# Optimization experiments

Hardware: AMD Instinct MI355X
Metric: run time of the kernel (lower is better)

Reference implementation:

```python
import jax, jax.numpy as jnp
import numpy as np

N_NODES = 50000
IN_F, HID_F, OUT_F = 256, 128, 40
N_EDGES = 800000


def _uniform(key, shape, scale):
    return jax.random.uniform(key, shape, dtype=jnp.float32, minval=-scale, maxval=scale)


def setup_inputs() -> dict:
    key = jax.random.key(0)
    ks = jax.random.split(key, 20)
    x = jax.random.normal(ks[0], (N_NODES, IN_F), dtype=jnp.float32)
    edge_index = jax.random.randint(ks[1], (2, N_EDGES), 0, N_NODES, dtype=jnp.int64)
    s0, sa0 = 1.0 / np.sqrt(HID_F), 1.0  # std_att = 1/sqrt(1)
    s1, sa1 = 1.0 / np.sqrt(OUT_F), 1.0
    sv = 1.0 / np.sqrt(3.0)
    return {
        "x": x, "edge_index": edge_index,
        "Wl0": _uniform(ks[2], (IN_F, HID_F), s0),
        "Wh0": _uniform(ks[3], (IN_F, HID_F), s0),
        "Wm0": _uniform(ks[4], (IN_F, HID_F), s0),
        "al0": _uniform(ks[5], (HID_F, 1), sa0),
        "ah0": _uniform(ks[6], (HID_F, 1), sa0),
        "am0": _uniform(ks[7], (HID_F, 1), sa0),
        "att0": _uniform(ks[8], (3, 3), sv),
        "Wl1": _uniform(ks[9], (HID_F, OUT_F), s1),
        "Wh1": _uniform(ks[10], (HID_F, OUT_F), s1),
        "Wm1": _uniform(ks[11], (HID_F, OUT_F), s1),
        "al1": _uniform(ks[12], (OUT_F, 1), sa1),
        "ah1": _uniform(ks[13], (OUT_F, 1), sa1),
        "am1": _uniform(ks[14], (OUT_F, 1), sa1),
        "att1": _uniform(ks[15], (3, 3), sv),
    }


def _acm_layer(x, row, col, d_inv, Wl, Wh, Wm, al, ah, am, att):
    n = x.shape[0]
    hl, hh, hm = x @ Wl, x @ Wh, x @ Wm
    # adj_low @ M  with adj_low = D^{-1}(I + A): gather sources, scatter-add to rows
    def low(M):
        return d_inv[:, None] * (M + jax.ops.segment_sum(M[col], row, num_segments=n))
    out_low = jax.nn.relu(low(hl))
    out_high = jax.nn.relu(hh - low(hh))  # adj_high = I - adj_low
    out_mlp = jax.nn.relu(hm)
    T = 3.0
    sig = jax.nn.sigmoid(jnp.concatenate([out_low @ al, out_high @ ah, out_mlp @ am], axis=1))  # [n,3]
    a = jax.nn.softmax((sig @ att) / T, axis=1)
    return 3.0 * (a[:, 0:1] * out_low + a[:, 1:2] * out_high + a[:, 2:3] * out_mlp)


def reference(x, edge_index, Wl0, Wh0, Wm0, al0, ah0, am0, att0,
              Wl1, Wh1, Wm1, al1, ah1, am1, att1):
    n = x.shape[0]
    row, col = edge_index[0], edge_index[1]
    deg = jax.ops.segment_sum(jnp.ones_like(row, dtype=jnp.float32), row, num_segments=n)
    rowsum = 1.0 + deg  # rowsum of I + A (duplicates counted, as in scipy)
    d_inv = jnp.where(rowsum > 0, 1.0 / rowsum, 0.0)
    h = _acm_layer(x, row, col, d_inv, Wl0, Wh0, Wm0, al0, ah0, am0, att0)
    out = _acm_layer(h, row, col, d_inv, Wl1, Wh1, Wm1, al1, ah1, am1, att1)
    return out
```

## Files before the change

kernel.cpp:

```cpp
#include <hip/hip_runtime.h>
#include <math.h>

#define N_NODES 50000
#define N_EDGES 800000
#define IN_F    256
#define HID_F   128
#define OUT_F   40
#define W0N     (3*HID_F)
#define W1N     (3*OUT_F)
#define NB      ((N_NODES + 255) / 256)

#define SEG     128
#define EPB     (N_EDGES / SEG)
#define NWORD   (N_NODES / 2)
#define WB      ((NWORD + 255) / 256)

#define XB   ((N_NODES * IN_F) / (256 * 16))
#define P0B  ((IN_F * W0N) / 256)
#define P1B  ((HID_F * W1N) / 256)
#define PREPB (XB + P0B + P1B)

typedef __attribute__((ext_vector_type(8))) unsigned short ushort8;
typedef __attribute__((ext_vector_type(4))) unsigned short ushort4v;
typedef __attribute__((ext_vector_type(8))) __bf16 bf16x8;
typedef __attribute__((ext_vector_type(4))) float f32x4;
typedef __attribute__((ext_vector_type(2))) float f32x2;

static __device__ __forceinline__ float sigmoidf_(float x) {
    return 1.0f / (1.0f + expf(-x));
}

static __device__ __forceinline__ unsigned short f2bf(float f) {
    unsigned u = __float_as_uint(f);
    u += 0x7FFFu + ((u >> 16) & 1u);
    return (unsigned short)(u >> 16);
}

static __device__ __forceinline__ float bflo(unsigned u) { return __uint_as_float(u << 16); }
static __device__ __forceinline__ float bfhi(unsigned u) { return __uint_as_float(u & 0xffff0000u); }
static __device__ __forceinline__ int rfl(int v) { return __builtin_amdgcn_readfirstlane(v); }


__global__ __launch_bounds__(256) void k_hist(
        const int* __restrict__ ei, unsigned* __restrict__ segHist,
        unsigned short* __restrict__ rank, unsigned* __restrict__ rc) {
    __shared__ unsigned hist[NWORD];
    int t = threadIdx.x, seg = blockIdx.x;
    for (int i = t; i < NWORD; i += 256) hist[i] = 0;
    __syncthreads();
    int base = seg * EPB;
    for (int k = t; k < EPB; k += 256) {
        int e = base + k;
        int r = ei[e];
        int c = ei[N_EDGES + e];
        unsigned old = atomicAdd(&hist[r >> 1], (r & 1) ? 0x10000u : 1u);
        unsigned lr = (r & 1) ? (old >> 16) : (old & 0xffffu);
        rank[e] = (unsigned short)lr;
        rc[e] = ((unsigned)r << 16) | (unsigned)c;
    }
    __syncthreads();
    unsigned* dst = segHist + (size_t)seg * NWORD;
    for (int i = t; i < NWORD; i += 256) dst[i] = hist[i];
}


__global__ __launch_bounds__(256) void k_scanseg(
        unsigned* __restrict__ segHist, int* __restrict__ rowPtr,
        float* __restrict__ dinv, int* __restrict__ blkTot) {
    __shared__ int s[256];
    int t = threadIdx.x;
    int w = blockIdx.x * 256 + t;
    int cum0 = 0, cum1 = 0;
    if (w < NWORD) {
        for (int sg = 0; sg < SEG; ++sg) {
            size_t idx = (size_t)sg * NWORD + w;
            unsigned h = segHist[idx];
            segHist[idx] = ((unsigned)cum1 << 16) | (unsigned)cum0;
            cum0 += (int)(h & 0xffffu);
            cum1 += (int)(h >> 16);
        }
    }
    int deg0 = cum0, deg1 = cum1;
    int pair = deg0 + deg1;
    s[t] = pair; __syncthreads();
    for (int d = 1; d < 256; d <<= 1) {
        int x = (t >= d) ? s[t - d] : 0;
        __syncthreads();
        s[t] += x;
        __syncthreads();
    }
    int basep = s[t] - pair;
    if (w < NWORD) {
        rowPtr[2 * w]     = basep;
        rowPtr[2 * w + 1] = basep + deg0;
        dinv[2 * w]     = 1.0f / (1.0f + (float)deg0);
        dinv[2 * w + 1] = 1.0f / (1.0f + (float)deg1);
    }
    if (t == 255) blkTot[blockIdx.x] = s[255];
}

__global__ void k_scan2(int* __restrict__ blk) {
    __shared__ int s[256];
    int t = threadIdx.x;
    int v = (t < WB) ? blk[t] : 0;
    s[t] = v; __syncthreads();
    for (int d = 1; d < 256; d <<= 1) {
        int x = (t >= d) ? s[t - d] : 0;
        __syncthreads();
        s[t] += x;
        __syncthreads();
    }
    if (t < WB) blk[t] = s[t] - v;
}

__global__ void k_scan3(const int* __restrict__ blkOff, int* __restrict__ rowPtr) {
    int t = threadIdx.x;
    int gid = blockIdx.x * 256 + t;
    if (gid < N_NODES) rowPtr[gid] += blkOff[gid >> 9];
    if (gid == 0) rowPtr[N_NODES] = N_EDGES;
}


__global__ __launch_bounds__(256) void k_prep(
        const float* __restrict__ x, unsigned short* __restrict__ xb,
        const float* __restrict__ Wl0, const float* __restrict__ Wh0,
        const float* __restrict__ Wm0, unsigned short* __restrict__ W0t,
        const float* __restrict__ Wl1, const float* __restrict__ Wh1,
        const float* __restrict__ Wm1, unsigned short* __restrict__ W1t) {
    int b = blockIdx.x, t = threadIdx.x;
    if (b < XB) {
        size_t idx = (size_t)b * 4096 + t * 16;
        float4 f0 = *(const float4*)(x + idx);
        float4 f1 = *(const float4*)(x + idx + 4);
        float4 f2 = *(const float4*)(x + idx + 8);
        float4 f3 = *(const float4*)(x + idx + 12);
        ushort8 u0, u1;
        u0[0]=f2bf(f0.x); u0[1]=f2bf(f0.y); u0[2]=f2bf(f0.z); u0[3]=f2bf(f0.w);
        u0[4]=f2bf(f1.x); u0[5]=f2bf(f1.y); u0[6]=f2bf(f1.z); u0[7]=f2bf(f1.w);
        u1[0]=f2bf(f2.x); u1[1]=f2bf(f2.y); u1[2]=f2bf(f2.z); u1[3]=f2bf(f2.w);
        u1[4]=f2bf(f3.x); u1[5]=f2bf(f3.y); u1[6]=f2bf(f3.z); u1[7]=f2bf(f3.w);
        *(ushort8*)(xb + idx)     = u0;
        *(ushort8*)(xb + idx + 8) = u1;
    } else if (b < XB + P0B) {
        int i = (b - XB) * 256 + t;
        int n = i / IN_F, k = i % IN_F;
        float v;
        if (n < HID_F)            v = Wl0[k * HID_F + n];
        else if (n < 2 * HID_F)   v = Wh0[k * HID_F + (n - HID_F)];
        else                      v = Wm0[k * HID_F + (n - 2 * HID_F)];
        W0t[i] = f2bf(v);
    } else {
        int i = (b - XB - P0B) * 256 + t;
        int n = i / HID_F, kp = i % HID_F;
        int k = ((kp >> 6) << 6) + ((kp & 3) << 4) + ((kp >> 2) & 15);
        float v;
        if (n < OUT_F)            v = Wl1[k * OUT_F + n];
        else if (n < 2 * OUT_F)   v = Wh1[k * OUT_F + (n - OUT_F)];
        else                      v = Wm1[k * OUT_F + (n - 2 * OUT_F)];
        W1t[i] = f2bf(v);
    }
}


#define BKP 40

template<int EPI>
__global__ __launch_bounds__(256) void k_gemm_fill(
        const unsigned short* __restrict__ A, const unsigned short* __restrict__ Bt,
        unsigned short* __restrict__ C0, int ld0,
        unsigned short* __restrict__ C1, int ld1, int nsplit,
        unsigned char* __restrict__ Cq,
        unsigned short* __restrict__ Hs, unsigned char* __restrict__ Hq,
        unsigned short* __restrict__ HmP,
        int M, int N, int K, int nxt,
        const unsigned* __restrict__ rc, const unsigned short* __restrict__ rank,
        const int* __restrict__ rowPtr, const unsigned short* __restrict__ segOff,
        unsigned short* __restrict__ colIdx) {
    __shared__ unsigned short As[128 * BKP];
    __shared__ unsigned short Bs[128 * BKP];
    int tid  = threadIdx.x;

    if ((int)blockIdx.x >= nxt) {
        int fid = (blockIdx.x - nxt) * gridDim.y + blockIdx.y;
        int e = fid * 256 + tid;
        if (e < N_EDGES) {
            unsigned x = rc[e];
            int r = (int)(x >> 16);
            int seg = e / EPB;
            int pos = rowPtr[r] + (int)segOff[(size_t)seg * N_NODES + r] + (int)rank[e];
            colIdx[pos] = (unsigned short)(x & 0xffffu);
        }
        return;
    }

    int lane = tid & 63, wid = tid >> 6;
    int wr = wid >> 1, wc = wid & 1;
    int bm = blockIdx.y * 128, bn = blockIdx.x * 128;

    int srow = tid >> 1;
    int scol = (tid & 1) * 16;

    int garow = min(bm + srow, M - 1);
    int gbrow = min(bn + srow, N - 1);

    f32x4 acc[4][4];
#pragma unroll
    for (int m = 0; m < 4; ++m)
#pragma unroll
        for (int n = 0; n < 4; ++n)
            acc[m][n] = (f32x4)(0.0f);

    int kg = (lane >> 4) * 8;
    int rA = wr * 64 + (lane & 15);
    int rB = wc * 64 + (lane & 15);

    for (int k0 = 0; k0 < K; k0 += 32) {
        {
            const unsigned short* src = A + (size_t)garow * K + k0 + scol;
            *(ushort8*)&As[srow * BKP + scol]     = *(const ushort8*)(src);
            *(ushort8*)&As[srow * BKP + scol + 8] = *(const ushort8*)(src + 8);
        }
        {
            const unsigned short* src = Bt + (size_t)gbrow * K + k0 + scol;
            *(ushort8*)&Bs[srow * BKP + scol]     = *(const ushort8*)(src);
            *(ushort8*)&Bs[srow * BKP + scol + 8] = *(const ushort8*)(src + 8);
        }
        __syncthreads();

        bf16x8 a[4], b[4];
#pragma unroll
        for (int m = 0; m < 4; ++m)
            a[m] = __builtin_bit_cast(bf16x8, *(const ushort8*)&As[(rA + m * 16) * BKP + kg]);
#pragma unroll
        for (int n = 0; n < 4; ++n)
            b[n] = __builtin_bit_cast(bf16x8, *(const ushort8*)&Bs[(rB + n * 16) * BKP + kg]);
#pragma unroll
        for (int m = 0; m < 4; ++m)
#pragma unroll
            for (int n = 0; n < 4; ++n)
                acc[m][n] = __builtin_amdgcn_mfma_f32_16x16x32_bf16(a[m], b[n], acc[m][n], 0, 0, 0);
        __syncthreads();
    }

    int col  = lane & 15;
    int rsub = (lane >> 4) * 4;

    if (EPI == 0) {
#pragma unroll
        for (int m = 0; m < 4; ++m) {
            int gm0 = bm + wr * 64 + m * 16 + rsub;
#pragma unroll
            for (int n = 0; n < 4; ++n) {
                int gn = bn + wc * 64 + n * 16 + col;
                if (gn >= N) continue;
#pragma unroll
                for (int j = 0; j < 4; ++j) {
                    int gm = gm0 + j;
                    if (gm >= M) continue;
                    float v = acc[m][n][j];
                    unsigned short b = f2bf(v);
                    if (gn < nsplit) {
                        C0[(size_t)gm * ld0 + gn] = b;
                        int pk = __builtin_amdgcn_cvt_pk_fp8_f32(v, v, 0, false);
                        Cq[(size_t)gm * nsplit + gn] = (unsigned char)(pk & 0xff);
                    } else {
                        C1[(size_t)gm * ld1 + (gn - nsplit)] = b;
                    }
                }
            }
        }
    } else {
#pragma unroll
        for (int m = 0; m < 4; ++m) {
            int gm0 = bm + wr * 64 + m * 16 + rsub;
#pragma unroll
            for (int j = 0; j < 4; ++j) {
                int gm = gm0 + j;
                if (gm >= M) continue;
                float v0 = acc[m][0][j], v1 = acc[m][1][j];
                float v2 = acc[m][2][j], v3 = acc[m][3][j];
                ushort4v o;
                o[0] = f2bf(v0); o[1] = f2bf(v1); o[2] = f2bf(v2); o[3] = f2bf(v3);
                if (bn < 256) {
                    int pos = bn + wc * 64 + col * 4;
                    *(ushort4v*)&Hs[(size_t)gm * 256 + pos] = o;
                    int pk = 0;
                    pk = __builtin_amdgcn_cvt_pk_fp8_f32(v0, v1, pk, false);
                    pk = __builtin_amdgcn_cvt_pk_fp8_f32(v2, v3, pk, true);
                    *(unsigned*)&Hq[(size_t)gm * 256 + pos] = (unsigned)pk;
                } else {
                    int pos = wc * 64 + col * 4;
                    *(ushort4v*)&HmP[(size_t)gm * 128 + pos] = o;
                }
            }
        }
    }
}


__global__ __launch_bounds__(256) void k_layer0(
        const unsigned short* __restrict__ Hs, const unsigned char* __restrict__ Hq,
        const unsigned short* __restrict__ HmP,
        const int* __restrict__ rowPtr, const unsigned short* __restrict__ colIdx,
        const float* __restrict__ dinv,
        const float* __restrict__ al, const float* __restrict__ ah,
        const float* __restrict__ am, const float* __restrict__ att,
        unsigned short* __restrict__ hout) {
    int lane = threadIdx.x & 63;
    int i = blockIdx.x * 4 + (threadIdx.x >> 6);

    int p0 = rfl(rowPtr[i]);
    int p1 = rfl(rowPtr[i + 1]);
    float a0 = 0.f, a1 = 0.f, a2 = 0.f, a3 = 0.f;
    int off4 = lane * 4;

    auto acc1 = [&](unsigned j) {
        const unsigned char* row = Hq + ((size_t)(j << 8));
        unsigned w = *(const unsigned*)(row + off4);
        f32x2 d0 = __builtin_amdgcn_cvt_pk_f32_fp8((int)w, false);
        f32x2 d1 = __builtin_amdgcn_cvt_pk_f32_fp8((int)w, true);
        a0 += d0.x; a1 += d0.y; a2 += d1.x; a3 += d1.y;
    };

    int p = p0;
    while ((p & 3) != 0 && p < p1) {
        acc1((unsigned)rfl((int)colIdx[p]));
        ++p;
    }
    for (; p + 7 < p1; p += 8) {
        uint2 ca = *(const uint2*)(colIdx + p);
        uint2 cb = *(const uint2*)(colIdx + p + 4);
        unsigned w0 = (unsigned)rfl((int)ca.x);
        unsigned w1 = (unsigned)rfl((int)ca.y);
        unsigned w2 = (unsigned)rfl((int)cb.x);
        unsigned w3 = (unsigned)rfl((int)cb.y);
        acc1(w0 & 0xffffu); acc1(w0 >> 16);
        acc1(w1 & 0xffffu); acc1(w1 >> 16);
        acc1(w2 & 0xffffu); acc1(w2 >> 16);
        acc1(w3 & 0xffffu); acc1(w3 >> 16);
    }
    for (; p + 3 < p1; p += 4) {
        uint2 ca = *(const uint2*)(colIdx + p);
        unsigned w0 = (unsigned)rfl((int)ca.x);
        unsigned w1 = (unsigned)rfl((int)ca.y);
        acc1(w0 & 0xffffu); acc1(w0 >> 16);
        acc1(w1 & 0xffffu); acc1(w1 >> 16);
    }
    for (; p < p1; ++p) {
        acc1((unsigned)rfl((int)colIdx[p]));
    }

    uint2 sv = *(const uint2*)(Hs + (size_t)i * 256 + off4);
    float s0 = bflo(sv.x), s1 = bfhi(sv.x), s2 = bflo(sv.y), s3 = bfhi(sv.y);
    float di = dinv[i];
    float l0 = di * (s0 + a0), l1 = di * (s1 + a1);
    float l2 = di * (s2 + a2), l3 = di * (s3 + a3);

    float ol0 = fmaxf(l0, 0.f), ol1 = fmaxf(l1, 0.f);
    float ol2 = fmaxf(l2, 0.f), ol3 = fmaxf(l3, 0.f);
    float oh0 = fmaxf(s0 - l0, 0.f), oh1 = fmaxf(s1 - l1, 0.f);
    float oh2 = fmaxf(s2 - l2, 0.f), oh3 = fmaxf(s3 - l3, 0.f);

    int c0 = ((lane >> 4) << 6) + (lane & 15);

    float om0 = 0.f, om1 = 0.f, om2 = 0.f, om3 = 0.f;
    float prA, prM = 0.f;
    if (lane < 32) {
        uint2 hv = *(const uint2*)(HmP + (size_t)i * 128 + off4);
        om0 = fmaxf(bflo(hv.x), 0.f); om1 = fmaxf(bfhi(hv.x), 0.f);
        om2 = fmaxf(bflo(hv.y), 0.f); om3 = fmaxf(bfhi(hv.y), 0.f);
        prA = ol0 * al[c0] + ol1 * al[c0 + 16] + ol2 * al[c0 + 32] + ol3 * al[c0 + 48];
        prM = om0 * am[c0] + om1 * am[c0 + 16] + om2 * am[c0 + 32] + om3 * am[c0 + 48];
    } else {
        int ch = c0 - 128;
        prA = oh0 * ah[ch] + oh1 * ah[ch + 16] + oh2 * ah[ch + 32] + oh3 * ah[ch + 48];
    }

#pragma unroll
    for (int d = 1; d < 32; d <<= 1) prA += __shfl_xor(prA, d);
#pragma unroll
    for (int d = 1; d < 32; d <<= 1) prM += __shfl_xor(prM, d);
    float g0 = __shfl(prA, 0);
    float g1 = __shfl(prA, 32);
    float g2 = __shfl(prM, 0);

    float sg0 = sigmoidf_(g0), sg1 = sigmoidf_(g1), sg2 = sigmoidf_(g2);
    const float inv3 = (1.0f / 3.0f);
    float e0 = (sg0 * att[0] + sg1 * att[3] + sg2 * att[6]) * inv3;
    float e1 = (sg0 * att[1] + sg1 * att[4] + sg2 * att[7]) * inv3;
    float e2 = (sg0 * att[2] + sg1 * att[5] + sg2 * att[8]) * inv3;
    float mx = fmaxf(e0, fmaxf(e1, e2));
    float x0 = expf(e0 - mx), x1 = expf(e1 - mx), x2 = expf(e2 - mx);
    float inv = 1.0f / (x0 + x1 + x2);
    float c0f = 3.0f * inv * x0, c1f = 3.0f * inv * x1, c2f = 3.0f * inv * x2;

    int src = lane | 32;
    float th0 = __shfl(oh0, src), th1 = __shfl(oh1, src);
    float th2 = __shfl(oh2, src), th3 = __shfl(oh3, src);

    if (lane < 32) {
        ushort4v o;
        o[0] = f2bf(c0f * ol0 + c1f * th0 + c2f * om0);
        o[1] = f2bf(c0f * ol1 + c1f * th1 + c2f * om1);
        o[2] = f2bf(c0f * ol2 + c1f * th2 + c2f * om2);
        o[3] = f2bf(c0f * ol3 + c1f * th3 + c2f * om3);
        *(ushort4v*)&hout[(size_t)i * 128 + off4] = o;
    }
}


__global__ __launch_bounds__(256) void k_layer1(
        const unsigned short* __restrict__ H1g, const unsigned char* __restrict__ H1q,
        const unsigned short* __restrict__ H1m,
        const int* __restrict__ rowPtr, const unsigned short* __restrict__ colIdx,
        const float* __restrict__ dinv,
        const float* __restrict__ al, const float* __restrict__ ah,
        const float* __restrict__ am, const float* __restrict__ att,
        float* __restrict__ out) {
    int lane = threadIdx.x & 63;
    int i = blockIdx.x * 4 + (threadIdx.x >> 6);

    int p0 = rfl(rowPtr[i]);
    int p1 = rfl(rowPtr[i + 1]);
    float a0 = 0.f, a1 = 0.f, a2 = 0.f, a3 = 0.f;
    int off4 = lane * 4;
    bool active = lane < 20;

    auto acc1 = [&](unsigned j) {
        const unsigned char* row = H1q + (size_t)(j * 80u);
        unsigned w = *(const unsigned*)(row + off4);
        f32x2 d0 = __builtin_amdgcn_cvt_pk_f32_fp8((int)w, false);
        f32x2 d1 = __builtin_amdgcn_cvt_pk_f32_fp8((int)w, true);
        a0 += d0.x; a1 += d0.y; a2 += d1.x; a3 += d1.y;
    };

    if (active) {
        int p = p0;
        while ((p & 3) != 0 && p < p1) {
            acc1((unsigned)rfl((int)colIdx[p]));
            ++p;
        }
        for (; p + 7 < p1; p += 8) {
            uint2 ca = *(const uint2*)(colIdx + p);
            uint2 cb = *(const uint2*)(colIdx + p + 4);
            unsigned w0 = (unsigned)rfl((int)ca.x);
            unsigned w1 = (unsigned)rfl((int)ca.y);
            unsigned w2 = (unsigned)rfl((int)cb.x);
            unsigned w3 = (unsigned)rfl((int)cb.y);
            acc1(w0 & 0xffffu); acc1(w0 >> 16);
            acc1(w1 & 0xffffu); acc1(w1 >> 16);
            acc1(w2 & 0xffffu); acc1(w2 >> 16);
            acc1(w3 & 0xffffu); acc1(w3 >> 16);
        }
        for (; p + 3 < p1; p += 4) {
            uint2 ca = *(const uint2*)(colIdx + p);
            unsigned w0 = (unsigned)rfl((int)ca.x);
            unsigned w1 = (unsigned)rfl((int)ca.y);
            acc1(w0 & 0xffffu); acc1(w0 >> 16);
            acc1(w1 & 0xffffu); acc1(w1 >> 16);
        }
        for (; p < p1; ++p) {
            acc1((unsigned)rfl((int)colIdx[p]));
        }
    }

    float s0 = 0.f, s1 = 0.f, s2 = 0.f, s3 = 0.f;
    if (active) {
        uint2 sv = *(const uint2*)(H1g + (size_t)i * 80 + off4);
        s0 = bflo(sv.x); s1 = bfhi(sv.x); s2 = bflo(sv.y); s3 = bfhi(sv.y);
    }
    float di = dinv[i];
    float l0 = di * (s0 + a0), l1 = di * (s1 + a1);
    float l2 = di * (s2 + a2), l3 = di * (s3 + a3);

    float ol0 = fmaxf(l0, 0.f), ol1 = fmaxf(l1, 0.f);
    float ol2 = fmaxf(l2, 0.f), ol3 = fmaxf(l3, 0.f);
    float oh0 = fmaxf(s0 - l0, 0.f), oh1 = fmaxf(s1 - l1, 0.f);
    float oh2 = fmaxf(s2 - l2, 0.f), oh3 = fmaxf(s3 - l3, 0.f);

    float om0 = 0.f, om1 = 0.f, om2 = 0.f, om3 = 0.f;
    float r0 = 0.f, r1 = 0.f, r2 = 0.f;
    if (lane < 10) {
        uint2 hv = *(const uint2*)(H1m + (size_t)i * 40 + off4);
        om0 = fmaxf(bflo(hv.x), 0.f); om1 = fmaxf(bfhi(hv.x), 0.f);
        om2 = fmaxf(bflo(hv.y), 0.f); om3 = fmaxf(bfhi(hv.y), 0.f);
        float4 alv = *(const float4*)(al + off4);
        float4 amv = *(const float4*)(am + off4);
        r0 = ol0 * alv.x + ol1 * alv.y + ol2 * alv.z + ol3 * alv.w;
        r2 = om0 * amv.x + om1 * amv.y + om2 * amv.z + om3 * amv.w;
    } else if (lane < 20) {
        float4 ahv = *(const float4*)(ah + (off4 - 40));
        r1 = oh0 * ahv.x + oh1 * ahv.y + oh2 * ahv.z + oh3 * ahv.w;
    }

#pragma unroll
    for (int d = 1; d < 64; d <<= 1) r0 += __shfl_xor(r0, d);
#pragma unroll
    for (int d = 1; d < 64; d <<= 1) r1 += __shfl_xor(r1, d);
#pragma unroll
    for (int d = 1; d < 64; d <<= 1) r2 += __shfl_xor(r2, d);

    float sg0 = sigmoidf_(r0), sg1 = sigmoidf_(r1), sg2 = sigmoidf_(r2);
    const float inv3 = (1.0f / 3.0f);
    float e0 = (sg0 * att[0] + sg1 * att[3] + sg2 * att[6]) * inv3;
    float e1 = (sg0 * att[1] + sg1 * att[4] + sg2 * att[7]) * inv3;
    float e2 = (sg0 * att[2] + sg1 * att[5] + sg2 * att[8]) * inv3;
    float mx = fmaxf(e0, fmaxf(e1, e2));
    float x0 = expf(e0 - mx), x1 = expf(e1 - mx), x2 = expf(e2 - mx);
    float inv = 1.0f / (x0 + x1 + x2);
    float c0 = 3.0f * inv * x0, c1 = 3.0f * inv * x1, c2 = 3.0f * inv * x2;

    int src = (lane + 10) & 63;
    float th0 = __shfl(oh0, src), th1 = __shfl(oh1, src);
    float th2 = __shfl(oh2, src), th3 = __shfl(oh3, src);

    if (lane < 10) {
        float4 o;
        o.x = c0 * ol0 + c1 * th0 + c2 * om0;
        o.y = c0 * ol1 + c1 * th1 + c2 * om1;
        o.z = c0 * ol2 + c1 * th2 + c2 * om2;
        o.w = c0 * ol3 + c1 * th3 + c2 * om3;
        *(float4*)&out[(size_t)i * 40 + off4] = o;
    }
}


extern "C" void kernel_launch(void* const* d_in, const int* in_sizes, int n_in,
                              void* d_out, int out_size, void* d_ws, size_t ws_size,
                              hipStream_t stream) {
    const float* x    = (const float*)d_in[0];
    const int*   ei   = (const int*)d_in[1];
    const float* Wl0  = (const float*)d_in[2];
    const float* Wh0  = (const float*)d_in[3];
    const float* Wm0  = (const float*)d_in[4];
    const float* al0  = (const float*)d_in[5];
    const float* ah0  = (const float*)d_in[6];
    const float* am0  = (const float*)d_in[7];
    const float* att0 = (const float*)d_in[8];
    const float* Wl1  = (const float*)d_in[9];
    const float* Wh1  = (const float*)d_in[10];
    const float* Wm1  = (const float*)d_in[11];
    const float* al1  = (const float*)d_in[12];
    const float* ah1  = (const float*)d_in[13];
    const float* am1  = (const float*)d_in[14];
    const float* att1 = (const float*)d_in[15];
    float* out = (float*)d_out;

    char* ws = (char*)d_ws;
    size_t off = 0;
    auto alloc = [&](size_t bytes) -> char* {
        char* p = ws + off;
        off += (bytes + 255) & ~(size_t)255;
        return p;
    };
    int*      rowPtr  = (int*)     alloc((size_t)(N_NODES + 1) * 4);
    int*      blkTot  = (int*)     alloc(256 * 4);
    unsigned* segHist = (unsigned*)alloc((size_t)SEG * NWORD * 4);
    unsigned short* rank   = (unsigned short*)alloc((size_t)N_EDGES * 2);
    unsigned*       rc     = (unsigned*)      alloc((size_t)N_EDGES * 4);
    unsigned short* colIdx = (unsigned short*)alloc((size_t)N_EDGES * 2);
    float* dinv   = (float*)alloc((size_t)N_NODES * 4);
    unsigned short* W0t  = (unsigned short*)alloc((size_t)W0N * IN_F * 2);
    unsigned short* W1t  = (unsigned short*)alloc((size_t)W1N * HID_F * 2);
    unsigned short* xb   = (unsigned short*)alloc((size_t)N_NODES * IN_F * 2);
    unsigned short* Hs   = (unsigned short*)alloc((size_t)N_NODES * 256 * 2);
    unsigned char*  Hq   = (unsigned char*) alloc((size_t)N_NODES * 256);
    unsigned short* HmP  = (unsigned short*)alloc((size_t)N_NODES * 128 * 2);
    unsigned short* H1g  = (unsigned short*)alloc((size_t)N_NODES * 80 * 2);
    unsigned char*  H1q  = (unsigned char*) alloc((size_t)N_NODES * 80 + 256);
    unsigned short* H1m  = (unsigned short*)alloc((size_t)N_NODES * 40 * 2);
    unsigned short* hbuf = (unsigned short*)alloc((size_t)N_NODES * HID_F * 2);

    k_hist<<<SEG, 256, 0, stream>>>(ei, segHist, rank, rc);
    k_prep<<<PREPB, 256, 0, stream>>>(x, xb, Wl0, Wh0, Wm0, W0t,
                                      Wl1, Wh1, Wm1, W1t);
    k_scanseg<<<WB, 256, 0, stream>>>(segHist, rowPtr, dinv, blkTot);
    k_scan2<<<1, 256, 0, stream>>>(blkTot);
    k_scan3<<<NB, 256, 0, stream>>>(blkTot, rowPtr);
    {
        dim3 grid(3 + 8, (N_NODES + 127) / 128);
        k_gemm_fill<1><<<grid, 256, 0, stream>>>(xb, W0t,
                                                 nullptr, 0, nullptr, 0, 0, nullptr,
                                                 Hs, Hq, HmP,
                                                 N_NODES, W0N, IN_F, 3,
                                                 rc, rank, rowPtr,
                                                 (const unsigned short*)segHist, colIdx);
    }
    k_layer0<<<N_NODES / 4, 256, 0, stream>>>(Hs, Hq, HmP, rowPtr, colIdx, dinv,
                                              al0, ah0, am0, att0, hbuf);
    {
        dim3 grid(1, (N_NODES + 127) / 128);
        k_gemm_fill<0><<<grid, 256, 0, stream>>>(hbuf, W1t,
                                                 H1g, 80, H1m, 40, 80, H1q,
                                                 nullptr, nullptr, nullptr,
                                                 N_NODES, W1N, HID_F, 1,
                                                 nullptr, nullptr, nullptr, nullptr, nullptr);
    }
    k_layer1<<<N_NODES / 4, 256, 0, stream>>>(H1g, H1q, H1m, rowPtr, colIdx, dinv,
                                              al1, ah1, am1, att1, out);
}
```

Measured before the change: 196.9 us.

## Fuse histogram and prep kernels; batch neighbor gathers via wave-wide shuffles

Merges the edge-histogram kernel and the bf16 conversion/weight-transpose kernel into one launch, using block-index ranges to pick the role. This removes a launch and lets the two independent stages run concurrently. The aggregation loops in both layer kernels now load up to 64 column indices per wave in one coalesced read and broadcast them with shuffles. Eight gathers are issued before any accumulation, which raises memory-level parallelism, and the layer-1 lane guard is dropped in favour of clamped offsets. The cost is that every block of the fused kernel reserves the large histogram shared array, which may sharply limit occupancy for the streaming conversion blocks.

Result: faster. 189.6 us (-3.7%).

```diff
diff --git a/kernel.cpp b/kernel.cpp
--- a/kernel.cpp
+++ b/kernel.cpp
@@ -18,7 +18,10 @@
 #define XB   ((N_NODES * IN_F) / (256 * 16))
 #define P0B  ((IN_F * W0N) / 256)
 #define P1B  ((HID_F * W1N) / 256)
-#define PREPB (XB + P0B + P1B)
+#define HPB0 (SEG)
+#define HPB1 (SEG + XB)
+#define HPB2 (SEG + XB + P0B)
+#define HPREPB (SEG + XB + P0B + P1B)
 
 typedef __attribute__((ext_vector_type(8))) unsigned short ushort8;
 typedef __attribute__((ext_vector_type(4))) unsigned short ushort4v;
@@ -41,26 +44,64 @@
 static __device__ __forceinline__ int rfl(int v) { return __builtin_amdgcn_readfirstlane(v); }
 
 
-__global__ __launch_bounds__(256) void k_hist(
+__global__ __launch_bounds__(256) void k_hp(
         const int* __restrict__ ei, unsigned* __restrict__ segHist,
-        unsigned short* __restrict__ rank, unsigned* __restrict__ rc) {
+        unsigned short* __restrict__ rank, unsigned* __restrict__ rc,
+        const float* __restrict__ x, unsigned short* __restrict__ xb,
+        const float* __restrict__ Wl0, const float* __restrict__ Wh0,
+        const float* __restrict__ Wm0, unsigned short* __restrict__ W0t,
+        const float* __restrict__ Wl1, const float* __restrict__ Wh1,
+        const float* __restrict__ Wm1, unsigned short* __restrict__ W1t) {
     __shared__ unsigned hist[NWORD];
-    int t = threadIdx.x, seg = blockIdx.x;
-    for (int i = t; i < NWORD; i += 256) hist[i] = 0;
-    __syncthreads();
-    int base = seg * EPB;
-    for (int k = t; k < EPB; k += 256) {
-        int e = base + k;
-        int r = ei[e];
-        int c = ei[N_EDGES + e];
-        unsigned old = atomicAdd(&hist[r >> 1], (r & 1) ? 0x10000u : 1u);
-        unsigned lr = (r & 1) ? (old >> 16) : (old & 0xffffu);
-        rank[e] = (unsigned short)lr;
-        rc[e] = ((unsigned)r << 16) | (unsigned)c;
-    }
-    __syncthreads();
-    unsigned* dst = segHist + (size_t)seg * NWORD;
-    for (int i = t; i < NWORD; i += 256) dst[i] = hist[i];
+    int b = blockIdx.x, t = threadIdx.x;
+    if (b < SEG) {
+        int seg = b;
+        for (int i = t; i < NWORD; i += 256) hist[i] = 0;
+        __syncthreads();
+        int base = seg * EPB;
+        for (int k = t; k < EPB; k += 256) {
+            int e = base + k;
+            int r = ei[e];
+            int c = ei[N_EDGES + e];
+            unsigned old = atomicAdd(&hist[r >> 1], (r & 1) ? 0x10000u : 1u);
+            unsigned lr = (r & 1) ? (old >> 16) : (old & 0xffffu);
+            rank[e] = (unsigned short)lr;
+            rc[e] = ((unsigned)r << 16) | (unsigned)c;
+        }
+        __syncthreads();
+        unsigned* dst = segHist + (size_t)seg * NWORD;
+        for (int i = t; i < NWORD; i += 256) dst[i] = hist[i];
+    } else if (b < HPB1) {
+        size_t idx = (size_t)(b - HPB0) * 4096 + t * 16;
+        float4 f0 = *(const float4*)(x + idx);
+        float4 f1 = *(const float4*)(x + idx + 4);
+        float4 f2 = *(const float4*)(x + idx + 8);
+        float4 f3 = *(const float4*)(x + idx + 12);
+        ushort8 u0, u1;
+        u0[0]=f2bf(f0.x); u0[1]=f2bf(f0.y); u0[2]=f2bf(f0.z); u0[3]=f2bf(f0.w);
+        u0[4]=f2bf(f1.x); u0[5]=f2bf(f1.y); u0[6]=f2bf(f1.z); u0[7]=f2bf(f1.w);
+        u1[0]=f2bf(f2.x); u1[1]=f2bf(f2.y); u1[2]=f2bf(f2.z); u1[3]=f2bf(f2.w);
+        u1[4]=f2bf(f3.x); u1[5]=f2bf(f3.y); u1[6]=f2bf(f3.z); u1[7]=f2bf(f3.w);
+        *(ushort8*)(xb + idx)     = u0;
+        *(ushort8*)(xb + idx + 8) = u1;
+    } else if (b < HPB2) {
+        int i = (b - HPB1) * 256 + t;
+        int n = i / IN_F, k = i % IN_F;
+        float v;
+        if (n < HID_F)            v = Wl0[k * HID_F + n];
+        else if (n < 2 * HID_F)   v = Wh0[k * HID_F + (n - HID_F)];
+        else                      v = Wm0[k * HID_F + (n - 2 * HID_F)];
+        W0t[i] = f2bf(v);
+    } else {
+        int i = (b - HPB2) * 256 + t;
+        int n = i / HID_F, kp = i % HID_F;
+        int k = ((kp >> 6) << 6) + ((kp & 3) << 4) + ((kp >> 2) & 15);
+        float v;
+        if (n < OUT_F)            v = Wl1[k * OUT_F + n];
+        else if (n < 2 * OUT_F)   v = Wh1[k * OUT_F + (n - OUT_F)];
+        else                      v = Wm1[k * OUT_F + (n - 2 * OUT_F)];
+        W1t[i] = f2bf(v);
+    }
 }
 
 
@@ -118,47 +159,6 @@
     int gid = blockIdx.x * 256 + t;
     if (gid < N_NODES) rowPtr[gid] += blkOff[gid >> 9];
     if (gid == 0) rowPtr[N_NODES] = N_EDGES;
-}
-
-
-__global__ __launch_bounds__(256) void k_prep(
-        const float* __restrict__ x, unsigned short* __restrict__ xb,
-        const float* __restrict__ Wl0, const float* __restrict__ Wh0,
-        const float* __restrict__ Wm0, unsigned short* __restrict__ W0t,
-        const float* __restrict__ Wl1, const float* __restrict__ Wh1,
-        const float* __restrict__ Wm1, unsigned short* __restrict__ W1t) {
-    int b = blockIdx.x, t = threadIdx.x;
-    if (b < XB) {
-        size_t idx = (size_t)b * 4096 + t * 16;
-        float4 f0 = *(const float4*)(x + idx);
-        float4 f1 = *(const float4*)(x + idx + 4);
-        float4 f2 = *(const float4*)(x + idx + 8);
-        float4 f3 = *(const float4*)(x + idx + 12);
-        ushort8 u0, u1;
-        u0[0]=f2bf(f0.x); u0[1]=f2bf(f0.y); u0[2]=f2bf(f0.z); u0[3]=f2bf(f0.w);
-        u0[4]=f2bf(f1.x); u0[5]=f2bf(f1.y); u0[6]=f2bf(f1.z); u0[7]=f2bf(f1.w);
-        u1[0]=f2bf(f2.x); u1[1]=f2bf(f2.y); u1[2]=f2bf(f2.z); u1[3]=f2bf(f2.w);
-        u1[4]=f2bf(f3.x); u1[5]=f2bf(f3.y); u1[6]=f2bf(f3.z); u1[7]=f2bf(f3.w);
-        *(ushort8*)(xb + idx)     = u0;
-        *(ushort8*)(xb + idx + 8) = u1;
-    } else if (b < XB + P0B) {
-        int i = (b - XB) * 256 + t;
-        int n = i / IN_F, k = i % IN_F;
-        float v;
-        if (n < HID_F)            v = Wl0[k * HID_F + n];
-        else if (n < 2 * HID_F)   v = Wh0[k * HID_F + (n - HID_F)];
-        else                      v = Wm0[k * HID_F + (n - 2 * HID_F)];
-        W0t[i] = f2bf(v);
-    } else {
-        int i = (b - XB - P0B) * 256 + t;
-        int n = i / HID_F, kp = i % HID_F;
-        int k = ((kp >> 6) << 6) + ((kp & 3) << 4) + ((kp >> 2) & 15);
-        float v;
-        if (n < OUT_F)            v = Wl1[k * OUT_F + n];
-        else if (n < 2 * OUT_F)   v = Wh1[k * OUT_F + (n - OUT_F)];
-        else                      v = Wm1[k * OUT_F + (n - 2 * OUT_F)];
-        W1t[i] = f2bf(v);
-    }
 }
 
 
@@ -311,43 +311,41 @@
 
     int p0 = rfl(rowPtr[i]);
     int p1 = rfl(rowPtr[i + 1]);
+    int deg = p1 - p0;
     float a0 = 0.f, a1 = 0.f, a2 = 0.f, a3 = 0.f;
     int off4 = lane * 4;
 
-    auto acc1 = [&](unsigned j) {
-        const unsigned char* row = Hq + ((size_t)(j << 8));
-        unsigned w = *(const unsigned*)(row + off4);
+    auto gath = [&](int js) -> unsigned {
+        return *(const unsigned*)(Hq + ((size_t)(unsigned)js << 8) + off4);
+    };
+    auto addw = [&](unsigned w) {
         f32x2 d0 = __builtin_amdgcn_cvt_pk_f32_fp8((int)w, false);
         f32x2 d1 = __builtin_amdgcn_cvt_pk_f32_fp8((int)w, true);
         a0 += d0.x; a1 += d0.y; a2 += d1.x; a3 += d1.y;
     };
 
-    int p = p0;
-    while ((p & 3) != 0 && p < p1) {
-        acc1((unsigned)rfl((int)colIdx[p]));
-        ++p;
-    }
-    for (; p + 7 < p1; p += 8) {
-        uint2 ca = *(const uint2*)(colIdx + p);
-        uint2 cb = *(const uint2*)(colIdx + p + 4);
-        unsigned w0 = (unsigned)rfl((int)ca.x);
-        unsigned w1 = (unsigned)rfl((int)ca.y);
-        unsigned w2 = (unsigned)rfl((int)cb.x);
-        unsigned w3 = (unsigned)rfl((int)cb.y);
-        acc1(w0 & 0xffffu); acc1(w0 >> 16);
-        acc1(w1 & 0xffffu); acc1(w1 >> 16);
-        acc1(w2 & 0xffffu); acc1(w2 >> 16);
-        acc1(w3 & 0xffffu); acc1(w3 >> 16);
-    }
-    for (; p + 3 < p1; p += 4) {
-        uint2 ca = *(const uint2*)(colIdx + p);
-        unsigned w0 = (unsigned)rfl((int)ca.x);
-        unsigned w1 = (unsigned)rfl((int)ca.y);
-        acc1(w0 & 0xffffu); acc1(w0 >> 16);
-        acc1(w1 & 0xffffu); acc1(w1 >> 16);
-    }
-    for (; p < p1; ++p) {
-        acc1((unsigned)rfl((int)colIdx[p]));
+    for (int c = 0; c < deg; c += 64) {
+        int rem = deg - c; if (rem > 64) rem = 64;
+        int mycol = (int)colIdx[p0 + c + (lane < rem ? lane : 0)];
+        int q = 0;
+        for (; q + 7 < rem; q += 8) {
+            int j0 = rfl(__shfl(mycol, q + 0));
+            int j1 = rfl(__shfl(mycol, q + 1));
+            int j2 = rfl(__shfl(mycol, q + 2));
+            int j3 = rfl(__shfl(mycol, q + 3));
+            int j4 = rfl(__shfl(mycol, q + 4));
+            int j5 = rfl(__shfl(mycol, q + 5));
+            int j6 = rfl(__shfl(mycol, q + 6));
+            int j7 = rfl(__shfl(mycol, q + 7));
+            unsigned w0 = gath(j0), w1 = gath(j1), w2 = gath(j2), w3 = gath(j3);
+            unsigned w4 = gath(j4), w5 = gath(j5), w6 = gath(j6), w7 = gath(j7);
+            addw(w0); addw(w1); addw(w2); addw(w3);
+            addw(w4); addw(w5); addw(w6); addw(w7);
+        }
+        for (; q < rem; ++q) {
+            int j = rfl(__shfl(mycol, q));
+            addw(gath(j));
+        }
     }
 
     uint2 sv = *(const uint2*)(Hs + (size_t)i * 256 + off4);
@@ -422,45 +420,42 @@
 
     int p0 = rfl(rowPtr[i]);
     int p1 = rfl(rowPtr[i + 1]);
+    int deg = p1 - p0;
     float a0 = 0.f, a1 = 0.f, a2 = 0.f, a3 = 0.f;
+    bool active = lane < 20;
     int off4 = lane * 4;
-    bool active = lane < 20;
-
-    auto acc1 = [&](unsigned j) {
-        const unsigned char* row = H1q + (size_t)(j * 80u);
-        unsigned w = *(const unsigned*)(row + off4);
+    int offc = active ? off4 : 0;
+
+    auto gath = [&](int js) -> unsigned {
+        return *(const unsigned*)(H1q + (size_t)((unsigned)js * 80u) + offc);
+    };
+    auto addw = [&](unsigned w) {
         f32x2 d0 = __builtin_amdgcn_cvt_pk_f32_fp8((int)w, false);
         f32x2 d1 = __builtin_amdgcn_cvt_pk_f32_fp8((int)w, true);
         a0 += d0.x; a1 += d0.y; a2 += d1.x; a3 += d1.y;
     };
 
-    if (active) {
-        int p = p0;
-        while ((p & 3) != 0 && p < p1) {
-            acc1((unsigned)rfl((int)colIdx[p]));
-            ++p;
-        }
-        for (; p + 7 < p1; p += 8) {
-            uint2 ca = *(const uint2*)(colIdx + p);
-            uint2 cb = *(const uint2*)(colIdx + p + 4);
-            unsigned w0 = (unsigned)rfl((int)ca.x);
-            unsigned w1 = (unsigned)rfl((int)ca.y);
-            unsigned w2 = (unsigned)rfl((int)cb.x);
-            unsigned w3 = (unsigned)rfl((int)cb.y);
-            acc1(w0 & 0xffffu); acc1(w0 >> 16);
-            acc1(w1 & 0xffffu); acc1(w1 >> 16);
-            acc1(w2 & 0xffffu); acc1(w2 >> 16);
-            acc1(w3 & 0xffffu); acc1(w3 >> 16);
-        }
-        for (; p + 3 < p1; p += 4) {
-            uint2 ca = *(const uint2*)(colIdx + p);
-            unsigned w0 = (unsigned)rfl((int)ca.x);
-            unsigned w1 = (unsigned)rfl((int)ca.y);
-            acc1(w0 & 0xffffu); acc1(w0 >> 16);
-            acc1(w1 & 0xffffu); acc1(w1 >> 16);
-        }
-        for (; p < p1; ++p) {
-            acc1((unsigned)rfl((int)colIdx[p]));
+    for (int c = 0; c < deg; c += 64) {
+        int rem = deg - c; if (rem > 64) rem = 64;
+        int mycol = (int)colIdx[p0 + c + (lane < rem ? lane : 0)];
+        int q = 0;
+        for (; q + 7 < rem; q += 8) {
+            int j0 = rfl(__shfl(mycol, q + 0));
+            int j1 = rfl(__shfl(mycol, q + 1));
+            int j2 = rfl(__shfl(mycol, q + 2));
+            int j3 = rfl(__shfl(mycol, q + 3));
+            int j4 = rfl(__shfl(mycol, q + 4));
+            int j5 = rfl(__shfl(mycol, q + 5));
+            int j6 = rfl(__shfl(mycol, q + 6));
+            int j7 = rfl(__shfl(mycol, q + 7));
+            unsigned w0 = gath(j0), w1 = gath(j1), w2 = gath(j2), w3 = gath(j3);
+            unsigned w4 = gath(j4), w5 = gath(j5), w6 = gath(j6), w7 = gath(j7);
+            addw(w0); addw(w1); addw(w2); addw(w3);
+            addw(w4); addw(w5); addw(w6); addw(w7);
+        }
+        for (; q < rem; ++q) {
+            int j = rfl(__shfl(mycol, q));
+            addw(gath(j));
         }
     }
 
@@ -558,7 +553,7 @@
     unsigned* segHist = (unsigned*)alloc((size_t)SEG * NWORD * 4);
     unsigned short* rank   = (unsigned short*)alloc((size_t)N_EDGES * 2);
     unsigned*       rc     = (unsigned*)      alloc((size_t)N_EDGES * 4);
-    unsigned short* colIdx = (unsigned short*)alloc((size_t)N_EDGES * 2);
+    unsigned short* colIdx = (unsigned short*)alloc((size_t)N_EDGES * 2 + 256);
     float* dinv   = (float*)alloc((size_t)N_NODES * 4);
     unsigned short* W0t  = (unsigned short*)alloc((size_t)W0N * IN_F * 2);
     unsigned short* W1t  = (unsigned short*)alloc((size_t)W1N * HID_F * 2);
@@ -571,9 +566,9 @@
     unsigned short* H1m  = (unsigned short*)alloc((size_t)N_NODES * 40 * 2);
     unsigned short* hbuf = (unsigned short*)alloc((size_t)N_NODES * HID_F * 2);
 
-    k_hist<<<SEG, 256, 0, stream>>>(ei, segHist, rank, rc);
-    k_prep<<<PREPB, 256, 0, stream>>>(x, xb, Wl0, Wh0, Wm0, W0t,
-                                      Wl1, Wh1, Wm1, W1t);
+    k_hp<<<HPREPB, 256, 0, stream>>>(ei, segHist, rank, rc,
+                                     x, xb, Wl0, Wh0, Wm0, W0t,
+                                     Wl1, Wh1, Wm1, W1t);
     k_scanseg<<<WB, 256, 0, stream>>>(segHist, rowPtr, dinv, blkTot);
     k_scan2<<<1, 256, 0, stream>>>(blkTot);
     k_scan3<<<NB, 256, 0, stream>>>(blkTot, rowPtr);
```
